# Kernel optimization log

Hardware: AMD Instinct MI355X
Metric: run time of the kernel (lower is better)

Reference implementation:

```python
import jax, jax.numpy as jnp
import numpy as np

N, HIDDEN, K = 16384, 256, 5  # k=5 neighbors, first (self) dropped -> 4 hyperedge memberships per node


def _knn_hyperedges(x):
    # Mimics sklearn NearestNeighbors(k=5) + drop self (torch code detaches x here).
    xs = jax.lax.stop_gradient(x)
    n = xs.shape[0]
    sq = jnp.sum(xs * xs, axis=1)
    d2 = sq[:, None] + sq[None, :] - 2.0 * (xs @ xs.T)  # [N, N] squared distances
    d2 = d2.at[jnp.arange(n), jnp.arange(n)].set(jnp.inf)  # exclude self
    _, idx = jax.lax.top_k(-d2, K - 1)  # [N, K-1] nearest neighbors
    node_idx = jnp.repeat(jnp.arange(n), K - 1)  # hyperedge_index[0]: node i
    edge_idx = idx.reshape(-1)                   # hyperedge_index[1]: hyperedge id = neighbor id
    return node_idx, edge_idx


def _prelu(x, a):
    return jnp.where(x >= 0, x, a * x)


def _hconv(x, W, b, node_idx, edge_idx, n):
    # PyG HypergraphConv (heads=1, no attention, unit hyperedge weights):
    # out = D^{-1} H B^{-1} H^T (x W^T) + b
    xt = x @ W.T  # lin has no bias in PyG; bias added at the end
    ones = jnp.ones(node_idx.shape[0], dtype=x.dtype)
    Bdeg = jax.ops.segment_sum(ones, edge_idx, num_segments=n)  # hyperedge degree
    Binv = jnp.where(Bdeg > 0, 1.0 / Bdeg, 0.0)
    Ddeg = jax.ops.segment_sum(ones, node_idx, num_segments=n)  # node degree
    Dinv = jnp.where(Ddeg > 0, 1.0 / Ddeg, 0.0)
    # node -> hyperedge gather/scatter
    e_feat = jax.ops.segment_sum(xt[node_idx], edge_idx, num_segments=n) * Binv[:, None]
    # hyperedge -> node gather/scatter
    out = jax.ops.segment_sum(e_feat[edge_idx], node_idx, num_segments=n) * Dinv[:, None]
    return out + b


def setup_inputs() -> dict:
    key = jax.random.key(0)
    k0, k1, k2, k3 = jax.random.split(key, 4)
    x = jax.random.normal(k0, (N, HIDDEN), dtype=jnp.float32)
    edge_index = jax.random.randint(k1, (2, 65536), 0, N)  # unused by the math, kept per signature
    kaiming = np.sqrt(2.0 / HIDDEN)
    W1 = jax.random.normal(k2, (HIDDEN, HIDDEN), dtype=jnp.float32) * kaiming
    W2 = jax.random.normal(k3, (HIDDEN, HIDDEN), dtype=jnp.float32) * kaiming
    b1 = jnp.zeros((HIDDEN,), dtype=jnp.float32)
    b2 = jnp.zeros((HIDDEN,), dtype=jnp.float32)
    prelu_a = jnp.float32(0.25)  # nn.PReLU() default single shared parameter
    return {"x": x, "edge_index": edge_index, "W1": W1, "b1": b1, "W2": W2, "b2": b2, "prelu_a": prelu_a}


def reference(x, edge_index, W1, b1, W2, b2, prelu_a):
    n = x.shape[0]
    node_idx, edge_idx = _knn_hyperedges(x)
    h = _hconv(x, W1, b1, node_idx, edge_idx, n)
    h = _prelu(h, prelu_a)
    h = _hconv(h, W2, b2, node_idx, edge_idx, n)
    h = h + x  # residual
    return _prelu(h, prelu_a)
```

## Files before the change

### kernel.cpp

```cpp
#include <hip/hip_runtime.h>
#include <stdint.h>

#define NN   16384
#define HID  256
#define LDSK 264
#define NSLICE 16
#define JSL  (NN/NSLICE)
#define JT   32
#define NIT  (JSL/JT)
#define NSETS 4
#define ITILE (NSETS*64)
#define NRS  8
#define GSB  2048
#define NWV  (GSB*4)
#define FLTMAX 3.402823466e38f
#define KEYMAX 0xFFFFFFFFu
#define VBIAS 131072.0f
#define MSTRIDE 17

typedef __attribute__((ext_vector_type(8))) _Float16 f16x8;
typedef __attribute__((ext_vector_type(4))) _Float16 f16x4;
typedef __attribute__((ext_vector_type(4))) float f32x4;

typedef const __attribute__((address_space(1))) unsigned int* gAS1;
typedef __attribute__((address_space(3))) unsigned int* lAS3;

#define NXG (NN*HID/4)
#define NWG (HID*HID/4)
#define CVTB ((NXG + 2*NWG)/256)
__global__ __launch_bounds__(256) void prep_kernel(const float* __restrict__ x,
                                                   const float* __restrict__ W1,
                                                   const float* __restrict__ W2,
                                                   _Float16* __restrict__ xh,
                                                   _Float16* __restrict__ W1h,
                                                   _Float16* __restrict__ W2h,
                                                   float* __restrict__ sqf,
                                                   int* __restrict__ Bdeg){
  #pragma clang fp contract(off)
  int b = blockIdx.x;
  int g0 = b * 256 + threadIdx.x;
  if (g0 < NN) Bdeg[g0] = 0;
  if (b < CVTB){
    int g = g0;
    const float* src; _Float16* dst; int o;
    if (g < NXG)            { src = x;  dst = xh;  o = g; }
    else if (g < NXG + NWG) { src = W1; dst = W1h; o = g - NXG; }
    else                    { src = W2; dst = W2h; o = g - NXG - NWG; }
    float4 v = ((const float4*)src)[o];
    f16x4 h; h.x = (_Float16)v.x; h.y = (_Float16)v.y; h.z = (_Float16)v.z; h.w = (_Float16)v.w;
    ((f16x4*)dst)[o] = h;
  } else {
    int bb = b - CVTB;
    int lane = threadIdx.x & 63;
    int rw   = lane >> 4;
    int h    = (lane >> 3) & 1;
    int j    = lane & 7;
    int row  = (bb * 4 + (threadIdx.x >> 6)) * 4 + rw;
    const float* p = x + (size_t)row * HID + h*128 + j;
    float v0 = p[0];
    float r  = v0 * v0;
    #pragma unroll
    for (int i = 1; i < 16; ++i){ float v = p[i*8]; float m = v * v; r = r + m; }
    float t1 = r  + __shfl_xor(r,  1);
    float t2 = t1 + __shfl_xor(t1, 2);
    float t3 = t2 + __shfl_xor(t2, 4);
    float tot = t3 + __shfl_xor(t3, 8);
    if (h == 0 && j == 0) sqf[row] = tot;
  }
}

__device__ __forceinline__ void load_tile64(unsigned short* dst, const unsigned short* src, int tid){
  const uint4* s = (const uint4*)src;
  #pragma unroll
  for (int r = 0; r < 8; ++r){
    int fl  = tid + (r << 8);
    int row = fl >> 5;
    int c   = fl & 31;
    *(uint4*)&dst[row*LDSK + (c << 3)] = s[fl];
  }
}

__device__ __forceinline__ unsigned umed3(unsigned a, unsigned b, unsigned c){
  unsigned d;
  asm("v_med3_u32 %0, %1, %2, %3" : "=v"(d) : "v"(a), "v"(b), "v"(c));
  return d;
}
__device__ __forceinline__ void ins4(unsigned (&b)[4], unsigned k){
  unsigned b0 = b[0], b1 = b[1], b2 = b[2];
  b[0] = k < b0 ? k : b0;
  b[1] = umed3(k, b0, b1);
  b[2] = umed3(k, b1, b2);
  b[3] = umed3(k, b2, b[3]);
}

__global__ __launch_bounds__(256, 2) void knn_kernel(const _Float16* __restrict__ xh,
                                                     const float* __restrict__ sqf,
                                                     unsigned* __restrict__ candk){
  __shared__ __align__(16) unsigned short Xj[2][JT*256];
  __shared__ __align__(16) float sqjA[JSL];

  int tid  = threadIdx.x;
  int sl   = blockIdx.x & (NSLICE-1);
  int i0   = (blockIdx.x / NSLICE) * ITILE;
  int jb0  = sl * JSL;
  int wave = tid >> 6, lane = tid & 63, quad = lane >> 4, lcol = lane & 15;

  f16x8 bfr[NSETS][8];
  #pragma unroll
  for (int s = 0; s < NSETS; ++s){
    const _Float16* br = xh + (size_t)(i0 + s*64 + wave*16 + lcol) * HID + quad*8;
    #pragma unroll
    for (int ks = 0; ks < 8; ++ks) bfr[s][ks] = *(const f16x8*)(br + ks*32);
  }

  const _Float16* gsrc[4];
  #pragma unroll
  for (int r = 0; r < 4; ++r){
    int m   = r*256 + tid;
    int row = m >> 5;
    int ch  = m & 31;
    gsrc[r] = xh + (size_t)row * HID + ((ch ^ (row & 7)) << 3);
  }

  int b0 = lcol*512 + ((quad ^ (lcol & 3)) << 4) + (((lcol >> 2) & 1) << 6);
  int b1 = b0 ^ 64;

  unsigned bk[NSETS][4];
  #pragma unroll
  for (int s = 0; s < NSETS; ++s)
    #pragma unroll
    for (int e = 0; e < 4; ++e) bk[s][e] = KEYMAX;

  {
    float4 sv = ((const float4*)(sqf + jb0))[tid];
    float4 sw;
    sw.x = fmaf(sv.x, 64.f, VBIAS); sw.y = fmaf(sv.y, 64.f, VBIAS);
    sw.z = fmaf(sv.z, 64.f, VBIAS); sw.w = fmaf(sv.w, 64.f, VBIAS);
    ((float4*)sqjA)[tid] = sw;
    size_t joff = (size_t)jb0 * HID;
    #pragma unroll
    for (int r = 0; r < 4; ++r)
      __builtin_amdgcn_global_load_lds((gAS1)(const void*)(gsrc[r] + joff),
                                       (lAS3)(void*)&Xj[0][(r*256 + tid) * 8],
                                       16, 0, 0);
    asm volatile("s_waitcnt vmcnt(0) lgkmcnt(0)" ::: "memory");
  }
  __builtin_amdgcn_s_barrier();
  __builtin_amdgcn_sched_barrier(0);

  for (int it = 0; it < NIT; ++it){
    int cur = it & 1;
    if (it + 1 < NIT){
      int nb = cur ^ 1;
      int jn = jb0 + (it + 1) * JT;
      size_t joff = (size_t)jn * HID;
      #pragma unroll
      for (int r = 0; r < 4; ++r)
        __builtin_amdgcn_global_load_lds((gAS1)(const void*)(gsrc[r] + joff),
                                         (lAS3)(void*)&Xj[nb][(r*256 + tid) * 8],
                                         16, 0, 0);
      asm volatile("s_waitcnt vmcnt(4)" ::: "memory");
    } else {
      asm volatile("s_waitcnt vmcnt(0)" ::: "memory");
    }
    __builtin_amdgcn_s_barrier();
    __builtin_amdgcn_sched_barrier(0);

    const char*  tb  = (const char*)&Xj[cur][0];
    const float* sjb = &sqjA[it * JT];
    int jb = jb0 + it * JT;

    #pragma unroll
    for (int sub = 0; sub < 2; ++sub){
      f32x4 acc[NSETS];
      #pragma unroll
      for (int s = 0; s < NSETS; ++s) acc[s] = (f32x4){0.f,0.f,0.f,0.f};
      #pragma unroll
      for (int ks = 0; ks < 8; ++ks){
        f16x8 a = *(const f16x8*)(tb + sub*8192 + ((ks >> 1) << 7) + ((ks & 1) ? b1 : b0));
        #pragma unroll
        for (int s = 0; s < NSETS; ++s)
          acc[s] = __builtin_amdgcn_mfma_f32_16x16x32_f16(a, bfr[s][ks], acc[s], 0, 0, 0);
      }
      float4 sj4 = *(const float4*)&sjb[sub*16 + quad*4];
      int jbase = jb + sub*16 + quad*4;
      #pragma unroll
      for (int reg = 0; reg < 4; ++reg){
        int gj = jbase + reg;
        float sj = (&sj4.x)[reg];
        #pragma unroll
        for (int s = 0; s < NSETS; ++s){
          float v64 = fmaf(-128.f, acc[s][reg], sj);
          unsigned kv = (unsigned)v64;
          unsigned key = (kv << 14) + (unsigned)gj;
          ins4(bk[s], key);
        }
      }
    }
    asm volatile("s_waitcnt lgkmcnt(0)" ::: "memory");
    __builtin_amdgcn_s_barrier();
    __builtin_amdgcn_sched_barrier(0);
  }

  unsigned* Mk = (unsigned*)Xj;
  #pragma unroll
  for (int s = 0; s < NSETS; ++s){
    int base = (s*64 + wave*16 + lcol)*MSTRIDE + quad*4;
    #pragma unroll
    for (int e = 0; e < 4; ++e) Mk[base+e] = bk[s][e];
  }
  __syncthreads();
  if (tid < ITILE){
    unsigned fk[4];
    #pragma unroll
    for (int e = 0; e < 4; ++e) fk[e] = KEYMAX;
    #pragma unroll
    for (int s = 0; s < 16; ++s) ins4(fk, Mk[tid*MSTRIDE + s]);
    int g = i0 + tid;
    #pragma unroll
    for (int e = 0; e < 4; ++e)
      candk[(size_t)g*(NSLICE*4) + sl*4 + e] = fk[e];
  }
}

__global__ __launch_bounds__(64) void rescore_kernel(const float* __restrict__ x,
                                                     const float* __restrict__ sqf,
                                                     const unsigned* __restrict__ candk,
                                                     int* __restrict__ idx_out,
                                                     int* __restrict__ Bdeg){
  #pragma clang fp contract(off)
  __shared__ unsigned Mk[8][65];
  __shared__ int   sel[8][8];
  __shared__ float dex[8][8];
  int t = threadIdx.x;
  int n = t >> 3, c = t & 7;
  int g = blockIdx.x * 8 + n;

  unsigned kr[8];
  {
    const uint4* kp = (const uint4*)(candk + (size_t)g*64 + c*8);
    uint4 k0 = kp[0], k1 = kp[1];
    kr[0]=k0.x; kr[1]=k0.y; kr[2]=k0.z; kr[3]=k0.w;
    kr[4]=k1.x; kr[5]=k1.y; kr[6]=k1.z; kr[7]=k1.w;
  }
  #pragma unroll
  for (int q = 0; q < 8; ++q)
    if ((kr[q] & 16383u) == (unsigned)g) kr[q] = KEYMAX;
  #pragma unroll
  for (int q = 0; q < 8; ++q) Mk[n][c*8+q] = kr[q];
  __syncthreads();

  int rank[8];
  #pragma unroll
  for (int q = 0; q < 8; ++q) rank[q] = 0;
  for (int s = 0; s < 64; ++s){
    unsigned ks = Mk[n][s];
    #pragma unroll
    for (int q = 0; q < 8; ++q) rank[q] += (ks < kr[q]) ? 1 : 0;
  }
  #pragma unroll
  for (int q = 0; q < 8; ++q)
    if (rank[q] < NRS) sel[n][rank[q]] = (int)(kr[q] & 16383u);
  __syncthreads();

  {
    int j = sel[n][c];
    const float4* xi = (const float4*)(x + (size_t)g * HID);
    const float4* xj = (const float4*)(x + (size_t)j * HID);
    float acc = 0.f;
    for (int k4 = 0; k4 < HID/4; ++k4){
      float4 a = xi[k4];
      float4 b = xj[k4];
      acc = fmaf(a.x, b.x, acc);
      acc = fmaf(a.y, b.y, acc);
      acc = fmaf(a.z, b.z, acc);
      acc = fmaf(a.w, b.w, acc);
    }
    float t1   = sqf[g] + sqf[j];
    float twod = 2.0f * acc;
    dex[n][c] = t1 - twod;
  }
  __syncthreads();

  if (c == 0){
    unsigned taken = 0;
    #pragma unroll
    for (int k = 0; k < 4; ++k){
      float bdv = FLTMAX; int bj = 0x7fffffff, bs = -1;
      for (int s = 0; s < NRS; ++s){
        if (taken & (1u << s)) continue;
        float d = dex[n][s]; int j = sel[n][s];
        if (d < bdv || (d == bdv && j < bj)){ bdv = d; bj = j; bs = s; }
      }
      taken |= 1u << bs;
      idx_out[g*4 + k] = bj;
      atomicAdd(&Bdeg[bj], 1);
    }
  }
}

__global__ __launch_bounds__(256) void gemm_xw(const _Float16* __restrict__ A,
                                               const _Float16* __restrict__ W,
                                               _Float16* __restrict__ out){
  __shared__ unsigned short Ws[64 * LDSK];
  int tid = threadIdx.x;
  int i0 = (blockIdx.x >> 2) * 64;
  int o0 = (blockIdx.x & 3)  * 64;
  int wave = tid >> 6, lane = tid & 63, quad = lane >> 4, lcol = lane & 15;
  load_tile64(Ws, (const unsigned short*)(W + (size_t)o0 * HID), tid);
  f16x8 a[8];
  const _Float16* arow = A + (size_t)(i0 + wave*16 + lcol) * HID + quad*8;
  #pragma unroll
  for (int ks = 0; ks < 8; ++ks) a[ks] = *(const f16x8*)(arow + ks*32);
  __syncthreads();
  #pragma unroll
  for (int sub = 0; sub < 4; ++sub){
    f32x4 acc = {0.f, 0.f, 0.f, 0.f};
    #pragma unroll
    for (int ks = 0; ks < 8; ++ks){
      f16x8 b = *(const f16x8*)&Ws[(sub*16 + lcol)*LDSK + quad*8 + ks*32];
      acc = __builtin_amdgcn_mfma_f32_16x16x32_f16(a[ks], b, acc, 0, 0, 0);
    }
    #pragma unroll
    for (int reg = 0; reg < 4; ++reg)
      out[(size_t)(i0 + wave*16 + quad*4 + reg)*HID + o0 + sub*16 + lcol] = (_Float16)acc[reg];
  }
}

__global__ __launch_bounds__(256) void prefix_kernel(const int* __restrict__ Bdeg,
                                                     int* __restrict__ off,
                                                     int* __restrict__ cursor){
  __shared__ int psum[256];
  __shared__ int excl[256];
  int t = threadIdx.x;
  int base = t * 64;
  int s = 0;
  for (int k = 0; k < 64; ++k) s += Bdeg[base + k];
  psum[t] = s;
  __syncthreads();
  if (t == 0){ int a = 0; for (int k = 0; k < 256; ++k){ excl[k] = a; a += psum[k]; } }
  __syncthreads();
  int a = excl[t];
  for (int k = 0; k < 64; ++k){ int dv = Bdeg[base + k]; off[base+k] = a; cursor[base+k] = a; a += dv; }
}

__global__ __launch_bounds__(256) void fill_kernel(const int* __restrict__ idx,
                                                   int* __restrict__ cursor,
                                                   int* __restrict__ rev){
  int i = blockIdx.x * 256 + threadIdx.x;
  #pragma unroll
  for (int t = 0; t < 4; ++t){
    int e = idx[i*4 + t];
    int p = atomicAdd(&cursor[e], 1);
    rev[p] = i;
  }
}

__global__ __launch_bounds__(256) void efeat_kernel(const _Float16* __restrict__ xt,
                                                    const int* __restrict__ off,
                                                    const int* __restrict__ deg,
                                                    const int* __restrict__ rev,
                                                    _Float16* __restrict__ E){
  int wv   = blockIdx.x * 4 + (threadIdx.x >> 6);
  int lane = threadIdx.x & 63;
  for (int e = wv; e < NN; e += NWV){
    int o = off[e], d = deg[e];
    float s0 = 0.f, s1 = 0.f, s2 = 0.f, s3 = 0.f;
    #pragma unroll 4
    for (int k = 0; k < d; ++k){
      int node = rev[o + k];
      f16x4 v = *(const f16x4*)(xt + (size_t)node * HID + lane * 4);
      s0 += (float)v.x; s1 += (float)v.y; s2 += (float)v.z; s3 += (float)v.w;
    }
    f16x4 w;
    if (d > 0){
      float fd = (float)d;
      w.x = (_Float16)(s0 / fd); w.y = (_Float16)(s1 / fd);
      w.z = (_Float16)(s2 / fd); w.w = (_Float16)(s3 / fd);
    } else {
      w.x = (_Float16)0.f; w.y = (_Float16)0.f; w.z = (_Float16)0.f; w.w = (_Float16)0.f;
    }
    *(f16x4*)(E + (size_t)e * HID + lane * 4) = w;
  }
}

__global__ __launch_bounds__(256) void fin1_kernel(const _Float16* __restrict__ E,
                                                   const int* __restrict__ idx,
                                                   const float* __restrict__ b1,
                                                   const float* __restrict__ pa,
                                                   _Float16* __restrict__ h1){
  int wv   = blockIdx.x * 4 + (threadIdx.x >> 6);
  int lane = threadIdx.x & 63;
  float4 bc = ((const float4*)b1)[lane];
  float a   = pa[0];
  for (int i = wv; i < NN; i += NWV){
    const int* ip = idx + i*4;
    int e0 = ip[0], e1 = ip[1], e2 = ip[2], e3 = ip[3];
    f16x4 v0 = *(const f16x4*)(E + (size_t)e0*HID + lane*4);
    f16x4 v1 = *(const f16x4*)(E + (size_t)e1*HID + lane*4);
    f16x4 v2 = *(const f16x4*)(E + (size_t)e2*HID + lane*4);
    f16x4 v3 = *(const f16x4*)(E + (size_t)e3*HID + lane*4);
    f16x4 w;
    #pragma unroll
    for (int c = 0; c < 4; ++c){
      float s = ((float)v0[c] + (float)v1[c] + (float)v2[c] + (float)v3[c]);
      float acc = 0.25f * s + (&bc.x)[c];
      acc = (acc >= 0.f) ? acc : a * acc;
      w[c] = (_Float16)acc;
    }
    *(f16x4*)(h1 + (size_t)i*HID + lane*4) = w;
  }
}

__global__ __launch_bounds__(256) void fin2_kernel(const _Float16* __restrict__ E,
                                                   const int* __restrict__ idx,
                                                   const float* __restrict__ b2,
                                                   const float* __restrict__ x,
                                                   const float* __restrict__ pa,
                                                   float* __restrict__ out){
  int wv   = blockIdx.x * 4 + (threadIdx.x >> 6);
  int lane = threadIdx.x & 63;
  float4 bc = ((const float4*)b2)[lane];
  float a   = pa[0];
  for (int i = wv; i < NN; i += NWV){
    const int* ip = idx + i*4;
    int e0 = ip[0], e1 = ip[1], e2 = ip[2], e3 = ip[3];
    f16x4 v0 = *(const f16x4*)(E + (size_t)e0*HID + lane*4);
    f16x4 v1 = *(const f16x4*)(E + (size_t)e1*HID + lane*4);
    f16x4 v2 = *(const f16x4*)(E + (size_t)e2*HID + lane*4);
    f16x4 v3 = *(const f16x4*)(E + (size_t)e3*HID + lane*4);
    float4 xr = *(const float4*)(x + (size_t)i*HID + lane*4);
    float4 w;
    #pragma unroll
    for (int c = 0; c < 4; ++c){
      float s = ((float)v0[c] + (float)v1[c] + (float)v2[c] + (float)v3[c]);
      float acc = 0.25f * s + (&bc.x)[c] + (&xr.x)[c];
      acc = (acc >= 0.f) ? acc : a * acc;
      (&w.x)[c] = acc;
    }
    *(float4*)(out + (size_t)i*HID + lane*4) = w;
  }
}

extern "C" void kernel_launch(void* const* d_in, const int* in_sizes, int n_in,
                              void* d_out, int out_size, void* d_ws, size_t ws_size,
                              hipStream_t stream){
  (void)in_sizes; (void)n_in; (void)out_size; (void)ws_size;
  const float* x  = (const float*)d_in[0];
  const float* W1 = (const float*)d_in[2];
  const float* b1 = (const float*)d_in[3];
  const float* W2 = (const float*)d_in[4];
  const float* b2 = (const float*)d_in[5];
  const float* pa = (const float*)d_in[6];
  float* out = (float*)d_out;

  char* ws = (char*)d_ws;
  float*  sqf    = (float*) (ws + 0);
  int*    idx    = (int*)   (ws + 65536);
  int*    Bdeg   = (int*)   (ws + 327680);
  int*    offE   = (int*)   (ws + 393216);
  int*    cursor = (int*)   (ws + 458752);
  int*    rev    = (int*)   (ws + 524288);
  _Float16* xh   = (_Float16*)(ws + (size_t)(5<<20));
  _Float16* W1h  = (_Float16*)(ws + (size_t)(13<<20));
  _Float16* W2h  = (_Float16*)(ws + (size_t)(13<<20) + 131072);
  _Float16* xt   = (_Float16*)(ws + (size_t)(13<<20) + 262144);
  _Float16* E    = (_Float16*)(ws + (size_t)(21<<20) + 262144);
  _Float16* h1   = (_Float16*)(ws + (size_t)(29<<20) + 262144);
  unsigned* candk = (unsigned*)xt;

  prep_kernel   <<<CVTB + NN/16, 256, 0, stream>>>(x, W1, W2, xh, W1h, W2h, sqf, Bdeg);
  knn_kernel    <<<(NN/ITILE)*NSLICE, 256, 0, stream>>>(xh, sqf, candk);
  rescore_kernel<<<NN/8, 64, 0, stream>>>(x, sqf, candk, idx, Bdeg);
  prefix_kernel <<<1, 256, 0, stream>>>(Bdeg, offE, cursor);
  fill_kernel   <<<NN/256, 256, 0, stream>>>(idx, cursor, rev);

  gemm_xw       <<<(NN/64)*4, 256, 0, stream>>>(xh, W1h, xt);
  efeat_kernel  <<<GSB, 256, 0, stream>>>(xt, offE, Bdeg, rev, E);
  fin1_kernel   <<<GSB, 256, 0, stream>>>(E, idx, b1, pa, h1);

  gemm_xw       <<<(NN/64)*4, 256, 0, stream>>>(h1, W2h, xt);
  efeat_kernel  <<<GSB, 256, 0, stream>>>(xt, offE, Bdeg, rev, E);
  fin2_kernel   <<<GSB, 256, 0, stream>>>(E, idx, b2, x, pa, out);
}
```

Measured before the change: 421.9 us.

## Fuse first XW GEMM into the kNN launch as extra tail blocks

```diff
diff --git a/kernel.cpp b/kernel.cpp
--- a/kernel.cpp
+++ b/kernel.cpp
@@ -13,6 +13,8 @@
 #define NRS  8
 #define GSB  2048
 #define NWV  (GSB*4)
+#define KNNB ((NN/ITILE)*NSLICE)
+#define GEMB ((NN/64)*4)
 #define FLTMAX 3.402823466e38f
 #define KEYMAX 0xFFFFFFFFu
 #define VBIAS 131072.0f
@@ -93,13 +95,49 @@
   b[3] = umed3(k, b2, b[3]);
 }
 
-__global__ __launch_bounds__(256, 2) void knn_kernel(const _Float16* __restrict__ xh,
-                                                     const float* __restrict__ sqf,
-                                                     unsigned* __restrict__ candk){
-  __shared__ __align__(16) unsigned short Xj[2][JT*256];
-  __shared__ __align__(16) float sqjA[JSL];
-
-  int tid  = threadIdx.x;
+__device__ __forceinline__ void gemm_body(const _Float16* __restrict__ A,
+                                          const _Float16* __restrict__ W,
+                                          _Float16* __restrict__ out,
+                                          unsigned short* Ws, int blk, int tid){
+  int i0 = (blk >> 2) * 64;
+  int o0 = (blk & 3)  * 64;
+  int wave = tid >> 6, lane = tid & 63, quad = lane >> 4, lcol = lane & 15;
+  load_tile64(Ws, (const unsigned short*)(W + (size_t)o0 * HID), tid);
+  f16x8 a[8];
+  const _Float16* arow = A + (size_t)(i0 + wave*16 + lcol) * HID + quad*8;
+  #pragma unroll
+  for (int ks = 0; ks < 8; ++ks) a[ks] = *(const f16x8*)(arow + ks*32);
+  __syncthreads();
+  #pragma unroll
+  for (int sub = 0; sub < 4; ++sub){
+    f32x4 acc = {0.f, 0.f, 0.f, 0.f};
+    #pragma unroll
+    for (int ks = 0; ks < 8; ++ks){
+      f16x8 b = *(const f16x8*)&Ws[(sub*16 + lcol)*LDSK + quad*8 + ks*32];
+      acc = __builtin_amdgcn_mfma_f32_16x16x32_f16(a[ks], b, acc, 0, 0, 0);
+    }
+    #pragma unroll
+    for (int reg = 0; reg < 4; ++reg)
+      out[(size_t)(i0 + wave*16 + quad*4 + reg)*HID + o0 + sub*16 + lcol] = (_Float16)acc[reg];
+  }
+}
+
+__global__ __launch_bounds__(256, 2) void knng_kernel(const _Float16* __restrict__ xh,
+                                                      const float* __restrict__ sqf,
+                                                      unsigned* __restrict__ candk,
+                                                      const _Float16* __restrict__ W1h,
+                                                      _Float16* __restrict__ xt){
+  __shared__ __align__(16) unsigned char smem[36864];
+
+  int tid = threadIdx.x;
+  if (blockIdx.x >= KNNB){
+    gemm_body(xh, W1h, xt, (unsigned short*)smem, blockIdx.x - KNNB, tid);
+    return;
+  }
+
+  unsigned short* XjB = (unsigned short*)smem;
+  float* sqjA = (float*)(smem + 32768);
+
   int sl   = blockIdx.x & (NSLICE-1);
   int i0   = (blockIdx.x / NSLICE) * ITILE;
   int jb0  = sl * JSL;
@@ -141,7 +179,7 @@
     #pragma unroll
     for (int r = 0; r < 4; ++r)
       __builtin_amdgcn_global_load_lds((gAS1)(const void*)(gsrc[r] + joff),
-                                       (lAS3)(void*)&Xj[0][(r*256 + tid) * 8],
+                                       (lAS3)(void*)&XjB[(r*256 + tid) * 8],
                                        16, 0, 0);
     asm volatile("s_waitcnt vmcnt(0) lgkmcnt(0)" ::: "memory");
   }
@@ -157,7 +195,7 @@
       #pragma unroll
       for (int r = 0; r < 4; ++r)
         __builtin_amdgcn_global_load_lds((gAS1)(const void*)(gsrc[r] + joff),
-                                         (lAS3)(void*)&Xj[nb][(r*256 + tid) * 8],
+                                         (lAS3)(void*)&XjB[(size_t)nb*JT*256 + (r*256 + tid) * 8],
                                          16, 0, 0);
       asm volatile("s_waitcnt vmcnt(4)" ::: "memory");
     } else {
@@ -166,7 +204,7 @@
     __builtin_amdgcn_s_barrier();
     __builtin_amdgcn_sched_barrier(0);
 
-    const char*  tb  = (const char*)&Xj[cur][0];
+    const char*  tb  = (const char*)&XjB[(size_t)cur*JT*256];
     const float* sjb = &sqjA[it * JT];
     int jb = jb0 + it * JT;
 
@@ -202,7 +240,7 @@
     __builtin_amdgcn_sched_barrier(0);
   }
 
-  unsigned* Mk = (unsigned*)Xj;
+  unsigned* Mk = (unsigned*)smem;
   #pragma unroll
   for (int s = 0; s < NSETS; ++s){
     int base = (s*64 + wave*16 + lcol)*MSTRIDE + quad*4;
@@ -303,28 +341,7 @@
                                                const _Float16* __restrict__ W,
                                                _Float16* __restrict__ out){
   __shared__ unsigned short Ws[64 * LDSK];
-  int tid = threadIdx.x;
-  int i0 = (blockIdx.x >> 2) * 64;
-  int o0 = (blockIdx.x & 3)  * 64;
-  int wave = tid >> 6, lane = tid & 63, quad = lane >> 4, lcol = lane & 15;
-  load_tile64(Ws, (const unsigned short*)(W + (size_t)o0 * HID), tid);
-  f16x8 a[8];
-  const _Float16* arow = A + (size_t)(i0 + wave*16 + lcol) * HID + quad*8;
-  #pragma unroll
-  for (int ks = 0; ks < 8; ++ks) a[ks] = *(const f16x8*)(arow + ks*32);
-  __syncthreads();
-  #pragma unroll
-  for (int sub = 0; sub < 4; ++sub){
-    f32x4 acc = {0.f, 0.f, 0.f, 0.f};
-    #pragma unroll
-    for (int ks = 0; ks < 8; ++ks){
-      f16x8 b = *(const f16x8*)&Ws[(sub*16 + lcol)*LDSK + quad*8 + ks*32];
-      acc = __builtin_amdgcn_mfma_f32_16x16x32_f16(a[ks], b, acc, 0, 0, 0);
-    }
-    #pragma unroll
-    for (int reg = 0; reg < 4; ++reg)
-      out[(size_t)(i0 + wave*16 + quad*4 + reg)*HID + o0 + sub*16 + lcol] = (_Float16)acc[reg];
-  }
+  gemm_body(A, W, out, Ws, blockIdx.x, threadIdx.x);
 }
 
 __global__ __launch_bounds__(256) void prefix_kernel(const int* __restrict__ Bdeg,
@@ -467,15 +484,14 @@
   _Float16* xt   = (_Float16*)(ws + (size_t)(13<<20) + 262144);
   _Float16* E    = (_Float16*)(ws + (size_t)(21<<20) + 262144);
   _Float16* h1   = (_Float16*)(ws + (size_t)(29<<20) + 262144);
-  unsigned* candk = (unsigned*)xt;
+  unsigned* candk = (unsigned*)E;
 
   prep_kernel   <<<CVTB + NN/16, 256, 0, stream>>>(x, W1, W2, xh, W1h, W2h, sqf, Bdeg);
-  knn_kernel    <<<(NN/ITILE)*NSLICE, 256, 0, stream>>>(xh, sqf, candk);
+  knng_kernel   <<<KNNB + GEMB, 256, 0, stream>>>(xh, sqf, candk, W1h, xt);
   rescore_kernel<<<NN/8, 64, 0, stream>>>(x, sqf, candk, idx, Bdeg);
   prefix_kernel <<<1, 256, 0, stream>>>(Bdeg, offE, cursor);
   fill_kernel   <<<NN/256, 256, 0, stream>>>(idx, cursor, rev);
 
-  gemm_xw       <<<(NN/64)*4, 256, 0, stream>>>(xh, W1h, xt);
   efeat_kernel  <<<GSB, 256, 0, stream>>>(xt, offE, Bdeg, rev, E);
   fin1_kernel   <<<GSB, 256, 0, stream>>>(E, idx, b1, pa, h1);
 
```

After: 407.8 us. -3.3%, faster.
